# Performance work log

Measured on AMD Instinct MI355X. Metric: run time of the kernel, lower is better.

## Reference

```python
import jax, jax.numpy as jnp
import numpy as np

BETA = 0.25


def setup_inputs() -> dict:
    key = jax.random.key(0)
    k1, k2 = jax.random.split(key)
    latents = jax.random.normal(k1, (16, 32, 32, 256), dtype=jnp.float32)
    codebook = jax.random.normal(k2, (8192, 256), dtype=jnp.float32) * 0.05
    return {"latents": latents, "codebook": codebook}


def reference(latents, codebook):
    # latents: [B, H, W, D]; codebook: [V, D]
    B, H, W, D = latents.shape
    flat = latents.reshape(-1, D)  # [N, D], N = B*H*W
    dist = (jnp.sum(flat * flat, axis=1, keepdims=True)
            + jnp.sum(codebook * codebook, axis=1)
            - 2.0 * jnp.einsum('nd,vd->nv', flat, codebook))  # [N, V]
    min_encoding_indices = jnp.argmin(dist, axis=1)  # [N]
    quantized = codebook[min_encoding_indices].reshape(B, H, W, D)
    sg = jax.lax.stop_gradient
    codebook_loss = (jnp.mean((sg(quantized) - latents) ** 2)
                     + BETA * jnp.mean((quantized - sg(latents)) ** 2))
    # straight-through estimator
    quantized_st = latents + sg(quantized - latents)
    return quantized_st, codebook_loss, min_encoding_indices
```

## Files before the change

### kernel.cpp

```cpp
#include <hip/hip_runtime.h>

#define N_ROWS 16384
#define DDIM   256
#define VCODES 8192
#define BETA   0.25f

using f16   = _Float16;
using f16x4 = __attribute__((ext_vector_type(4))) _Float16;
using f16x8 = __attribute__((ext_vector_type(8))) _Float16;
using f32x4 = __attribute__((ext_vector_type(4))) float;

typedef __attribute__((address_space(1))) const unsigned int gu32_t;
typedef __attribute__((address_space(3))) unsigned int       lu32_t;

__device__ __forceinline__ void gload16(const void* g, void* l) {
    __builtin_amdgcn_global_load_lds((gu32_t*)g, (lu32_t*)l, 16, 0, 0);
}


__global__ void split_lat(const float* __restrict__ lat, f16* __restrict__ Ap) {
    int t = blockIdx.x * 256 + threadIdx.x;
    float4 x = *(const float4*)&lat[(size_t)t * 4];
    int row = t >> 6;
    int c   = (t & 63) * 4;
    f16 h0 = (f16)x.x, h1 = (f16)x.y, h2 = (f16)x.z, h3 = (f16)x.w;
    f16 l0 = (f16)(x.x - (float)h0), l1 = (f16)(x.y - (float)h1);
    f16 l2 = (f16)(x.z - (float)h2), l3 = (f16)(x.w - (float)h3);
    f16x4 hi = {h0, h1, h2, h3}, lo = {l0, l1, l2, l3};
    int kt  = c >> 5;
    int sub = ((c & 31) >> 3) * 128 + (row & 15) * 8 + (c & 7);
    size_t base = ((size_t)(row >> 4) * 16);
    *(f16x4*)&Ap[(base + kt)     * 512 + sub] = hi;
    *(f16x4*)&Ap[(base + kt + 8) * 512 + sub] = lo;
}

__global__ void split_cb(const float* __restrict__ cb, f16* __restrict__ Bp) {
    int t = blockIdx.x * 256 + threadIdx.x;
    float4 e = *(const float4*)&cb[(size_t)t * 4];
    float ex = e.x * 64.0f, ey = e.y * 64.0f, ez = e.z * 64.0f, ew = e.w * 64.0f;
    int row = t >> 6;
    int c   = (t & 63) * 4;
    f16 h0 = (f16)ex, h1 = (f16)ey, h2 = (f16)ez, h3 = (f16)ew;
    f16 l0 = (f16)(ex - (float)h0), l1 = (f16)(ey - (float)h1);
    f16 l2 = (f16)(ez - (float)h2), l3 = (f16)(ew - (float)h3);
    f16x4 hi = {h0, h1, h2, h3}, lo = {l0, l1, l2, l3};
    int kt  = c >> 5;
    int sub = ((c & 31) >> 3) * 128 + (row & 15) * 8 + (c & 7);
    size_t base = ((size_t)(row >> 4) * 16);
    *(f16x4*)&Bp[(base + kt)     * 512 + sub] = hi;
    *(f16x4*)&Bp[(base + kt + 8) * 512 + sub] = lo;
}

__global__ void cbnorm_k(const float* __restrict__ cb, float* __restrict__ cbnorm) {
    int gtid = blockIdx.x * blockDim.x + threadIdx.x;
    int wave = gtid >> 6;
    int lane = threadIdx.x & 63;
    if (wave >= VCODES) return;
    float4 v = *(const float4*)(cb + (size_t)wave * DDIM + lane * 4);
    float s = v.x * v.x + v.y * v.y + v.z * v.z + v.w * v.w;
    #pragma unroll
    for (int m = 32; m; m >>= 1) s += __shfl_xor(s, m, 64);
    if (lane == 0) cbnorm[wave] = s;
}

__global__ __launch_bounds__(256, 2)
void vq_mfma(const f16* __restrict__ Ap, const f16* __restrict__ Bp,
             const float* __restrict__ cbn,
             float* __restrict__ pmin, int* __restrict__ pidx) {
    __shared__ __align__(16) f16 As[2][16 * 512];
    __shared__ __align__(16) f16 Bs[2][16 * 512];

    const int tid  = threadIdx.x;
    const int lane = tid & 63;
    const int w    = tid >> 6;
    const int wr   = w >> 1, wc = w & 1;
    const int l15  = lane & 15;
    const int l4   = lane >> 4;
    const int r0   = blockIdx.x * 128;
    const int vgrp = blockIdx.y;

    const char* Ag = (const char*)Ap + (size_t)(r0 >> 4) * 16384;
    const char* Bp0 = (const char*)Bp;

    auto stage = [&](int vt_, int vc_, int b) {
        const int akt = (vc_ < 8) ? (vc_ & 3) * 2 : 8 + (vc_ - 8) * 2;
        const int bkt = (vc_ < 4) ? vc_ * 2 : (vc_ < 8) ? 8 + (vc_ - 4) * 2 : (vc_ - 8) * 2;
        const char* Bg = Bp0 + (size_t)((vgrp * 512 + vt_ * 128) >> 4) * 16384;
        #pragma unroll
        for (int i = 0; i < 4; i++) {
            const int off = i * 4096 + tid * 16;
            const int s   = off >> 11;
            const int h   = (off >> 10) & 1;
            const int win = off & 1023;
            gload16(Ag + ((size_t)s * 16 + (akt + h)) * 1024 + win, (char*)As[b] + off);
        }
        #pragma unroll
        for (int i = 0; i < 4; i++) {
            const int off = i * 4096 + tid * 16;
            const int s   = off >> 11;
            const int h   = (off >> 10) & 1;
            const int win = off & 1023;
            gload16(Bg + ((size_t)s * 16 + (bkt + h)) * 1024 + win, (char*)Bs[b] + off);
        }
    };

    float rmin[4][4];
    int   ridx[4][4];
    #pragma unroll
    for (int m = 0; m < 4; m++)
        #pragma unroll
        for (int r = 0; r < 4; r++) { rmin[m][r] = 3.4e38f; ridx[m][r] = 0x7fffffff; }

    stage(0, 0, 0);

    for (int vt = 0; vt < 4; vt++) {
        const int v0 = vgrp * 512 + vt * 128;

        f32x4 acc[4][4];
        #pragma unroll
        for (int m = 0; m < 4; m++)
            #pragma unroll
            for (int n = 0; n < 4; n++) acc[m][n] = (f32x4){0.f, 0.f, 0.f, 0.f};

        for (int vc = 0; vc < 12; vc++) {
            const int cc = vt * 12 + vc;
            const int b  = cc & 1;
            __syncthreads();
            if (cc < 47) {
                const int nvt = (vc == 11) ? vt + 1 : vt;
                const int nvc = (vc == 11) ? 0 : vc + 1;
                stage(nvt, nvc, (cc + 1) & 1);
            }
            #pragma unroll
            for (int h = 0; h < 2; h++) {
                f16x8 af[4], bf[4];
                #pragma unroll
                for (int m = 0; m < 4; m++)
                    af[m] = *(const f16x8*)(As[b] + ((wr * 4 + m) * 2 + h) * 512 + lane * 8);
                #pragma unroll
                for (int n = 0; n < 4; n++)
                    bf[n] = *(const f16x8*)(Bs[b] + ((wc * 4 + n) * 2 + h) * 512 + lane * 8);
                #pragma unroll
                for (int m = 0; m < 4; m++)
                    #pragma unroll
                    for (int n = 0; n < 4; n++)
                        acc[m][n] = __builtin_amdgcn_mfma_f32_16x16x32_f16(af[m], bf[n], acc[m][n], 0, 0, 0);
            }
        }

        #pragma unroll
        for (int n = 0; n < 4; n++) {
            const int c = v0 + wc * 64 + n * 16 + l15;
            const float cn = cbn[c];
            #pragma unroll
            for (int m = 0; m < 4; m++)
                #pragma unroll
                for (int r = 0; r < 4; r++) {
                    float s = cn - acc[m][n][r] * 0.03125f;
                    if (s < rmin[m][r] || (s == rmin[m][r] && c < ridx[m][r])) {
                        rmin[m][r] = s; ridx[m][r] = c;
                    }
                }
        }
    }

    #pragma unroll
    for (int m = 0; m < 4; m++)
        #pragma unroll
        for (int r = 0; r < 4; r++) {
            float mv = rmin[m][r];
            int   id = ridx[m][r];
            #pragma unroll
            for (int o = 1; o < 16; o <<= 1) {
                float om = __shfl_xor(mv, o, 64);
                int  oid = __shfl_xor(id, o, 64);
                if (om < mv || (om == mv && oid < id)) { mv = om; id = oid; }
            }
            if (l15 == 0) {
                const int grow = r0 + wr * 64 + m * 16 + l4 * 4 + r;
                pmin[grow * 32 + vgrp * 2 + wc] = mv;
                pidx[grow * 32 + vgrp * 2 + wc] = id;
            }
        }
}

__global__ void combine_k(const float* __restrict__ lat, const float* __restrict__ cb,
                          const float* __restrict__ pmin, const int* __restrict__ pidx,
                          float* __restrict__ out_q, float* __restrict__ out_idx,
                          float* __restrict__ loss_part) {
    const int tid = threadIdx.x, lane = tid & 63, wv = tid >> 6;
    const int row = blockIdx.x * 4 + wv;

    float m = 3.4e38f; int id = 0x7fffffff;
    if (lane < 32) { m = pmin[row * 32 + lane]; id = pidx[row * 32 + lane]; }
    #pragma unroll
    for (int o = 32; o; o >>= 1) {
        float om = __shfl_xor(m, o, 64);
        int  oid = __shfl_xor(id, o, 64);
        if (om < m || (om == m && oid < id)) { m = om; id = oid; }
    }

    float4 q = *(const float4*)&cb[(size_t)id * DDIM + lane * 4];
    float4 x = *(const float4*)&lat[(size_t)row * DDIM + lane * 4];
    *(float4*)&out_q[(size_t)row * DDIM + lane * 4] = q;
    if (lane == 0) out_idx[row] = (float)id;

    float dx = q.x - x.x, dy = q.y - x.y, dz = q.z - x.z, dw = q.w - x.w;
    float s = dx * dx + dy * dy + dz * dz + dw * dw;
    #pragma unroll
    for (int o = 32; o; o >>= 1) s += __shfl_xor(s, o, 64);

    __shared__ float red[4];
    if (lane == 0) red[wv] = s;
    __syncthreads();
    if (tid == 0) loss_part[blockIdx.x] = red[0] + red[1] + red[2] + red[3];
}

__global__ void loss_k(const float* __restrict__ part, float* __restrict__ out_loss) {
    float s = 0.0f;
    for (int i = threadIdx.x; i < N_ROWS / 4; i += 256) s += part[i];
    #pragma unroll
    for (int m = 32; m; m >>= 1) s += __shfl_xor(s, m, 64);
    __shared__ float wsum[4];
    int lane = threadIdx.x & 63, w = threadIdx.x >> 6;
    if (lane == 0) wsum[w] = s;
    __syncthreads();
    if (threadIdx.x == 0) {
        float t = wsum[0] + wsum[1] + wsum[2] + wsum[3];
        *out_loss = (1.0f + BETA) * t / (float)((size_t)N_ROWS * DDIM);
    }
}

extern "C" void kernel_launch(void* const* d_in, const int* in_sizes, int n_in,
                              void* d_out, int out_size, void* d_ws, size_t ws_size,
                              hipStream_t stream) {
    const float* lat = (const float*)d_in[0];
    const float* cb  = (const float*)d_in[1];

    float* ws = (float*)d_ws;
    f16*   Ap       = (f16*)ws;
    f16*   Bp       = (f16*)(ws + 4194304);
    float* cbn      = ws + 4194304 + 2097152;
    float* pmin     = cbn + VCODES;
    int*   pidx     = (int*)(pmin + N_ROWS * 32);
    float* losspart = (float*)(pidx + N_ROWS * 32);

    float* out_q    = (float*)d_out;
    float* out_loss = out_q + (size_t)N_ROWS * DDIM;
    float* out_idx  = out_loss + 1;

    split_lat<<<N_ROWS * DDIM / 1024, 256, 0, stream>>>(lat, Ap);
    split_cb<<<VCODES * DDIM / 1024, 256, 0, stream>>>(cb, Bp);
    cbnorm_k<<<VCODES / 4, 256, 0, stream>>>(cb, cbn);

    dim3 grid(N_ROWS / 128, VCODES / 512);
    vq_mfma<<<grid, 256, 0, stream>>>(Ap, Bp, cbn, pmin, pidx);

    combine_k<<<N_ROWS / 4, 256, 0, stream>>>(lat, cb, pmin, pidx,
                                              out_q, out_idx, losspart);
    loss_k<<<1, 256, 0, stream>>>(losspart, out_loss);
}
```

Baseline: 312.9 us.

## Enlarge VQ MFMA tile to 256x256 with 8 waves and swizzled grid

The distance GEMM kernel moves from 128-row by 512-code blocks of 4 waves (each iterating over four 128-code sub-tiles) to 256x256 output tiles per 512-thread block, with each wave holding an 8x4 grid of MFMA accumulators. Block IDs are swizzled into a 1D grid to improve L2 reuse of A and B panels. The argmin is reduced across the four column waves through LDS before one partial per block is written, and s_setprio is raised around the MFMA burst. Larger tiles cut global/LDS traffic per FLOP but raise register pressure (128 accumulator VGPRs) and may lower occupancy.

```diff
diff --git a/kernel.cpp b/kernel.cpp
--- a/kernel.cpp
+++ b/kernel.cpp
@@ -63,125 +63,126 @@
     if (lane == 0) cbnorm[wave] = s;
 }
 
-__global__ __launch_bounds__(256, 2)
+__global__ __launch_bounds__(512, 2)
 void vq_mfma(const f16* __restrict__ Ap, const f16* __restrict__ Bp,
              const float* __restrict__ cbn,
              float* __restrict__ pmin, int* __restrict__ pidx) {
-    __shared__ __align__(16) f16 As[2][16 * 512];
-    __shared__ __align__(16) f16 Bs[2][16 * 512];
+    __shared__ __align__(16) f16 L[2][16384];
 
     const int tid  = threadIdx.x;
     const int lane = tid & 63;
     const int w    = tid >> 6;
-    const int wr   = w >> 1, wc = w & 1;
+    const int wr   = w >> 2;
+    const int wc   = w & 3;
     const int l15  = lane & 15;
     const int l4   = lane >> 4;
-    const int r0   = blockIdx.x * 128;
-    const int vgrp = blockIdx.y;
-
-    const char* Ag = (const char*)Ap + (size_t)(r0 >> 4) * 16384;
-    const char* Bp0 = (const char*)Bp;
-
-    auto stage = [&](int vt_, int vc_, int b) {
-        const int akt = (vc_ < 8) ? (vc_ & 3) * 2 : 8 + (vc_ - 8) * 2;
-        const int bkt = (vc_ < 4) ? vc_ * 2 : (vc_ < 8) ? 8 + (vc_ - 4) * 2 : (vc_ - 8) * 2;
-        const char* Bg = Bp0 + (size_t)((vgrp * 512 + vt_ * 128) >> 4) * 16384;
-        #pragma unroll
-        for (int i = 0; i < 4; i++) {
-            const int off = i * 4096 + tid * 16;
-            const int s   = off >> 11;
-            const int h   = (off >> 10) & 1;
+
+    const int id  = blockIdx.x;
+    const int swz = (id & 7) * 256 + (id >> 3);
+    const int bx  = swz & 63;
+    const int by  = swz >> 6;
+
+    const char* Ag = (const char*)Ap + (size_t)bx * 262144;
+    const char* Bg = (const char*)Bp + (size_t)by * 262144;
+
+    auto stage = [&](int vk, int b) {
+        const int akt = (vk < 8) ? vk : vk - 8;
+        const int bkt = (vk < 16) ? vk : vk - 16;
+        #pragma unroll
+        for (int i = 0; i < 2; i++) {
+            const int off = i * 8192 + tid * 16;
+            const int s   = off >> 10;
             const int win = off & 1023;
-            gload16(Ag + ((size_t)s * 16 + (akt + h)) * 1024 + win, (char*)As[b] + off);
-        }
-        #pragma unroll
-        for (int i = 0; i < 4; i++) {
-            const int off = i * 4096 + tid * 16;
-            const int s   = off >> 11;
-            const int h   = (off >> 10) & 1;
+            gload16(Ag + (size_t)(s * 16 + akt) * 1024 + win, (char*)&L[b][0] + off);
+        }
+        #pragma unroll
+        for (int i = 0; i < 2; i++) {
+            const int off = i * 8192 + tid * 16;
+            const int s   = off >> 10;
             const int win = off & 1023;
-            gload16(Bg + ((size_t)s * 16 + (bkt + h)) * 1024 + win, (char*)Bs[b] + off);
+            gload16(Bg + (size_t)(s * 16 + bkt) * 1024 + win, (char*)&L[b][0] + 16384 + off);
         }
     };
 
-    float rmin[4][4];
-    int   ridx[4][4];
-    #pragma unroll
-    for (int m = 0; m < 4; m++)
-        #pragma unroll
-        for (int r = 0; r < 4; r++) { rmin[m][r] = 3.4e38f; ridx[m][r] = 0x7fffffff; }
-
-    stage(0, 0, 0);
-
-    for (int vt = 0; vt < 4; vt++) {
-        const int v0 = vgrp * 512 + vt * 128;
-
-        f32x4 acc[4][4];
-        #pragma unroll
-        for (int m = 0; m < 4; m++)
+    f32x4 acc[8][4];
+    #pragma unroll
+    for (int m = 0; m < 8; m++)
+        #pragma unroll
+        for (int n = 0; n < 4; n++) acc[m][n] = (f32x4){0.f, 0.f, 0.f, 0.f};
+
+    stage(0, 0);
+    int cur = 0;
+
+    for (int vk = 0; vk < 24; vk++) {
+        __syncthreads();
+        if (vk < 23) stage(vk + 1, cur ^ 1);
+
+        const f16* Abase = &L[cur][0]    + (wr * 8) * 512;
+        const f16* Bbase = &L[cur][8192] + (wc * 4) * 512;
+
+        f16x8 bf[4], af[8];
+        #pragma unroll
+        for (int n = 0; n < 4; n++) bf[n] = *(const f16x8*)(Bbase + n * 512 + lane * 8);
+        #pragma unroll
+        for (int mm = 0; mm < 8; mm++) af[mm] = *(const f16x8*)(Abase + mm * 512 + lane * 8);
+
+        __builtin_amdgcn_s_setprio(1);
+        #pragma unroll
+        for (int mm = 0; mm < 8; mm++)
             #pragma unroll
-            for (int n = 0; n < 4; n++) acc[m][n] = (f32x4){0.f, 0.f, 0.f, 0.f};
-
-        for (int vc = 0; vc < 12; vc++) {
-            const int cc = vt * 12 + vc;
-            const int b  = cc & 1;
-            __syncthreads();
-            if (cc < 47) {
-                const int nvt = (vc == 11) ? vt + 1 : vt;
-                const int nvc = (vc == 11) ? 0 : vc + 1;
-                stage(nvt, nvc, (cc + 1) & 1);
-            }
-            #pragma unroll
-            for (int h = 0; h < 2; h++) {
-                f16x8 af[4], bf[4];
-                #pragma unroll
-                for (int m = 0; m < 4; m++)
-                    af[m] = *(const f16x8*)(As[b] + ((wr * 4 + m) * 2 + h) * 512 + lane * 8);
-                #pragma unroll
-                for (int n = 0; n < 4; n++)
-                    bf[n] = *(const f16x8*)(Bs[b] + ((wc * 4 + n) * 2 + h) * 512 + lane * 8);
-                #pragma unroll
-                for (int m = 0; m < 4; m++)
-                    #pragma unroll
-                    for (int n = 0; n < 4; n++)
-                        acc[m][n] = __builtin_amdgcn_mfma_f32_16x16x32_f16(af[m], bf[n], acc[m][n], 0, 0, 0);
-            }
-        }
-
+            for (int n = 0; n < 4; n++)
+                acc[mm][n] = __builtin_amdgcn_mfma_f32_16x16x32_f16(af[mm], bf[n], acc[mm][n], 0, 0, 0);
+        __builtin_amdgcn_s_setprio(0);
+
+        cur ^= 1;
+    }
+
+    float* sMin = (float*)&L[0][0];
+    int*   sIdx = (int*)((char*)&L[0][0] + 4096);
+
+    #pragma unroll
+    for (int m = 0; m < 8; m++) {
+        float rmin[4]; int ridx[4];
+        #pragma unroll
+        for (int r = 0; r < 4; r++) { rmin[r] = 3.4e38f; ridx[r] = 0x7fffffff; }
         #pragma unroll
         for (int n = 0; n < 4; n++) {
-            const int c = v0 + wc * 64 + n * 16 + l15;
+            const int c = by * 256 + wc * 64 + n * 16 + l15;
             const float cn = cbn[c];
             #pragma unroll
-            for (int m = 0; m < 4; m++)
-                #pragma unroll
-                for (int r = 0; r < 4; r++) {
-                    float s = cn - acc[m][n][r] * 0.03125f;
-                    if (s < rmin[m][r] || (s == rmin[m][r] && c < ridx[m][r])) {
-                        rmin[m][r] = s; ridx[m][r] = c;
-                    }
-                }
-        }
-    }
-
-    #pragma unroll
-    for (int m = 0; m < 4; m++)
+            for (int r = 0; r < 4; r++) {
+                float s = cn - acc[m][n][r] * 0.03125f;
+                if (s < rmin[r] || (s == rmin[r] && c < ridx[r])) { rmin[r] = s; ridx[r] = c; }
+            }
+        }
         #pragma unroll
         for (int r = 0; r < 4; r++) {
-            float mv = rmin[m][r];
-            int   id = ridx[m][r];
+            float mv = rmin[r]; int idv = ridx[r];
             #pragma unroll
             for (int o = 1; o < 16; o <<= 1) {
                 float om = __shfl_xor(mv, o, 64);
-                int  oid = __shfl_xor(id, o, 64);
-                if (om < mv || (om == mv && oid < id)) { mv = om; id = oid; }
+                int  oid = __shfl_xor(idv, o, 64);
+                if (om < mv || (om == mv && oid < idv)) { mv = om; idv = oid; }
             }
             if (l15 == 0) {
-                const int grow = r0 + wr * 64 + m * 16 + l4 * 4 + r;
-                pmin[grow * 32 + vgrp * 2 + wc] = mv;
-                pidx[grow * 32 + vgrp * 2 + wc] = id;
+                const int rloc = wr * 128 + m * 16 + l4 * 4 + r;
+                sMin[wc * 256 + rloc] = mv;
+                sIdx[wc * 256 + rloc] = idv;
             }
         }
+    }
+    __syncthreads();
+
+    if (tid < 256) {
+        float mv = sMin[tid]; int idv = sIdx[tid];
+        #pragma unroll
+        for (int j = 1; j < 4; j++) {
+            float om = sMin[j * 256 + tid]; int oid = sIdx[j * 256 + tid];
+            if (om < mv || (om == mv && oid < idv)) { mv = om; idv = oid; }
+        }
+        pmin[(bx * 256 + tid) * 32 + by] = mv;
+        pidx[(bx * 256 + tid) * 32 + by] = idv;
+    }
 }
 
 __global__ void combine_k(const float* __restrict__ lat, const float* __restrict__ cb,
@@ -253,8 +254,7 @@
     split_cb<<<VCODES * DDIM / 1024, 256, 0, stream>>>(cb, Bp);
     cbnorm_k<<<VCODES / 4, 256, 0, stream>>>(cb, cbn);
 
-    dim3 grid(N_ROWS / 128, VCODES / 512);
-    vq_mfma<<<grid, 256, 0, stream>>>(Ap, Bp, cbn, pmin, pidx);
+    vq_mfma<<<2048, 512, 0, stream>>>(Ap, Bp, cbn, pmin, pidx);
 
     combine_k<<<N_ROWS / 4, 256, 0, stream>>>(lat, cb, pmin, pidx,
                                               out_q, out_idx, losspart);
```

Measured after the change: 322.8 us. 3.2% more time.
